# Optimization experiments

Measured on AMD Instinct MI355X. Metric: run time of the kernel, lower is better.

The kernel has to match this reference:

```python
import jax, jax.numpy as jnp
import numpy as np

B, T, D, H = 8, 2048, 512, 2048
EPS = 1e-5


def setup_inputs() -> dict:
    key = jax.random.key(0)
    ks = jax.random.split(key, 12)
    s_d = 1.0 / np.sqrt(D)
    s_h = 1.0 / np.sqrt(H)
    s_w = np.sqrt(6.0 / (T + T))  # xavier_uniform scale for w [T,T]
    return {
        "x": jax.random.normal(ks[0], (B, T, D), jnp.float32),
        "ln1_g": jnp.ones((D,), jnp.float32),
        "ln1_b": jnp.zeros((D,), jnp.float32),
        "Wk": jax.random.normal(ks[1], (D, D), jnp.float32) * s_d,
        "bk": jnp.zeros((D,), jnp.float32),
        "Wv": jax.random.normal(ks[2], (D, D), jnp.float32) * s_d,
        "bv": jnp.zeros((D,), jnp.float32),
        "Wq": jax.random.normal(ks[3], (D, D), jnp.float32) * s_d,
        "bq": jnp.zeros((D,), jnp.float32),
        "w": jax.random.uniform(ks[4], (T, T), jnp.float32, -s_w, s_w),
        "Wo": jax.random.normal(ks[5], (D, D), jnp.float32) * s_d,
        "bo": jnp.zeros((D,), jnp.float32),
        "ln2_g": jnp.ones((D,), jnp.float32),
        "ln2_b": jnp.zeros((D,), jnp.float32),
        "W1": jax.random.normal(ks[6], (D, H), jnp.float32) * s_d,
        "b1": jnp.zeros((H,), jnp.float32),
        "W2": jax.random.normal(ks[7], (H, D), jnp.float32) * s_h,
        "b2": jnp.zeros((D,), jnp.float32),
    }


def _ln(x, g, b):
    mu = jnp.mean(x, axis=-1, keepdims=True)
    var = jnp.mean(jnp.square(x - mu), axis=-1, keepdims=True)
    return (x - mu) * jax.lax.rsqrt(var + EPS) * g + b


def _aft_full(h, Wk, bk, Wv, bv, Wq, bq, w, Wo, bo):
    # h: [B,T,D]
    K = h @ Wk + bk
    V = h @ Wv + bv
    # row-max stabilized position bias [T,T]
    exp_w = jnp.exp(w - jnp.max(w, axis=-1, keepdims=True))
    # NOTE: original stabilizes K with max over dim=0 (the BATCH dim) -- faithful
    exp_K = jnp.exp(K - jnp.max(K, axis=0, keepdims=True))  # [B,T,D]
    num = jnp.einsum("ts,bsd->btd", exp_w, exp_K * V)
    den = jnp.einsum("ts,bsd->btd", exp_w, exp_K)
    Yt = num / den
    Q = h @ Wq + bq
    Yt = jax.nn.sigmoid(Q) * Yt
    return Yt @ Wo + bo


def reference(x, ln1_g, ln1_b, Wk, bk, Wv, bv, Wq, bq, w, Wo, bo,
              ln2_g, ln2_b, W1, b1, W2, b2):
    attn = _aft_full(_ln(x, ln1_g, ln1_b), Wk, bk, Wv, bv, Wq, bq, w, Wo, bo)
    out = attn + x
    h = _ln(out, ln2_g, ln2_b)
    h = jax.nn.gelu(h @ W1 + b1, approximate=False)
    h = jax.nn.gelu(h @ W2 + b2, approximate=False)  # GELU after 2nd linear too (faithful)
    return h + out
```

## Files before the change

### kernel.cpp

```cpp
#include <hip/hip_runtime.h>
#include <hip/hip_bf16.h>
#include <math.h>

typedef __hip_bfloat16 bf16;
typedef __bf16 bf16x8 __attribute__((ext_vector_type(8)));
typedef float f32x4 __attribute__((ext_vector_type(4)));

#define B_ 8
#define T_ 2048
#define D_ 512
#define H_ 2048

__device__ __forceinline__ float b2f(unsigned short u) {
    return __uint_as_float((unsigned)u << 16);
}
__device__ __forceinline__ float ldf(const float* p, long i) { return p[i]; }
__device__ __forceinline__ float ldf(const bf16* p, long i) {
    return b2f(((const unsigned short*)p)[i]);
}
__device__ __forceinline__ float gelu_f(float v) {
    float a = 1.5957691216057308f * (v + 0.044715f * v * v * v);
    return v / (1.0f + __expf(-a));
}

__device__ __forceinline__ long poff(int row, int col, int K) {
    return ((long)(row >> 4) * (K >> 5) + (col >> 5)) * 512 + (row & 15) * 32 + (col & 31);
}

#define GLD16(g, l)                                                          \
    __builtin_amdgcn_global_load_lds(                                        \
        (const __attribute__((address_space(1))) void*)(g),                  \
        (__attribute__((address_space(3))) void*)(l), 16, 0, 0)

template <typename Tin, bool PACKO>
__global__ __launch_bounds__(256) void ln_kernel(const Tin* __restrict__ x,
                                                 const float* __restrict__ g,
                                                 const float* __restrict__ bb,
                                                 bf16* __restrict__ y) {
    int row = blockIdx.x;
    long base = (long)row * D_;
    int tid = threadIdx.x;
    float v0 = ldf(x, base + tid);
    float v1 = ldf(x, base + tid + 256);
    float s = v0 + v1;
#pragma unroll
    for (int off = 32; off > 0; off >>= 1) s += __shfl_down(s, off);
    __shared__ float red[4];
    int lane = tid & 63, wid = tid >> 6;
    if (lane == 0) red[wid] = s;
    __syncthreads();
    float mean = (red[0] + red[1] + red[2] + red[3]) * (1.0f / 512.0f);
    __syncthreads();
    float d0 = v0 - mean, d1 = v1 - mean;
    float vs = d0 * d0 + d1 * d1;
#pragma unroll
    for (int off = 32; off > 0; off >>= 1) vs += __shfl_down(vs, off);
    if (lane == 0) red[wid] = vs;
    __syncthreads();
    float var = (red[0] + red[1] + red[2] + red[3]) * (1.0f / 512.0f);
    float rstd = rsqrtf(var + 1e-5f);
    float o0 = d0 * rstd * g[tid] + bb[tid];
    float o1 = d1 * rstd * g[tid + 256] + bb[tid + 256];
    if (PACKO) {
        y[poff(row, tid, D_)]       = __float2bfloat16(o0);
        y[poff(row, tid + 256, D_)] = __float2bfloat16(o1);
    } else {
        y[base + tid]       = __float2bfloat16(o0);
        y[base + tid + 256] = __float2bfloat16(o1);
    }
}

__global__ __launch_bounds__(256) void expw_kernel(const float* __restrict__ w,
                                                   bf16* __restrict__ ew) {
    int row = blockIdx.x;
    long base = (long)row * T_;
    int tid = threadIdx.x;
    float v[8];
    float mx = -3.4e38f;
#pragma unroll
    for (int i = 0; i < 8; ++i) {
        v[i] = w[base + tid + i * 256];
        mx = fmaxf(mx, v[i]);
    }
#pragma unroll
    for (int off = 32; off > 0; off >>= 1) mx = fmaxf(mx, __shfl_down(mx, off));
    __shared__ float red[4];
    if ((tid & 63) == 0) red[tid >> 6] = mx;
    __syncthreads();
    float rmax = fmaxf(fmaxf(red[0], red[1]), fmaxf(red[2], red[3]));
#pragma unroll
    for (int i = 0; i < 8; ++i)
        ew[poff(row, tid + i * 256, T_)] = __float2bfloat16(expf(v[i] - rmax));
}

__global__ __launch_bounds__(256) void maxk_kernel(const bf16* __restrict__ K,
                                                   float* __restrict__ mk) {
    long i = (long)blockIdx.x * 256 + threadIdx.x;
    float m = ldf(K, i);
#pragma unroll
    for (int b = 1; b < B_; ++b) m = fmaxf(m, ldf(K, (long)b * (T_ * D_) + i));
    mk[i] = m;
}

__global__ __launch_bounds__(256) void kv2t_kernel(const bf16* __restrict__ K_,
                                                   const bf16* __restrict__ V_,
                                                   const float* __restrict__ mk,
                                                   bf16* __restrict__ kv2t) {
    __shared__ float sev[64][65];
    __shared__ float se[64][65];
    int tx = threadIdx.x & 63, ty = threadIdx.x >> 6;
    int t0 = blockIdx.x * 64, d0 = blockIdx.y * 64, b = blockIdx.z;
    long ibase = (long)b << 20;
#pragma unroll
    for (int r = 0; r < 16; ++r) {
        int tl = r * 4 + ty;
        long mi = (long)(t0 + tl) * D_ + d0 + tx;
        float e = expf(ldf(K_, ibase + mi) - mk[mi]);
        sev[tl][tx] = e * ldf(V_, ibase + mi);
        se[tl][tx] = e;
    }
    __syncthreads();
    long obase = (long)b << 21;
#pragma unroll
    for (int r = 0; r < 16; ++r) {
        int dl = r * 4 + ty;
        kv2t[obase + poff(d0 + dl, t0 + tx, T_)]       = __float2bfloat16(sev[tx][dl]);
        kv2t[obase + poff(512 + d0 + dl, t0 + tx, T_)] = __float2bfloat16(se[tx][dl]);
    }
}

__global__ __launch_bounds__(256) void yt_kernel(const bf16* __restrict__ nd,
                                                 bf16* __restrict__ q) {
    long i = (long)blockIdx.x * 256 + threadIdx.x;
    long td = i & (long)(T_ * D_ - 1);
    long b = i >> 20;
    long t = td >> 9;
    long d = td & (D_ - 1);
    long base = (b << 21) + (t << 10);
    float num = ldf(nd, base + d), den = ldf(nd, base + D_ + d);
    q[i] = __float2bfloat16(ldf(q, i) * num / den);
}

struct WT6 {
    const float* src[6];
    bf16* dst[6];
    int K[6], N[6];
};
__global__ __launch_bounds__(256) void wtrans6_kernel(WT6 p) {
    int z = blockIdx.z;
    int K = p.K[z], N = p.N[z];
    int n0 = blockIdx.x * 64, k0 = blockIdx.y * 64;
    if (n0 >= N || k0 >= K) return;
    const float* W = p.src[z];
    bf16* WT = p.dst[z];
    __shared__ float s[64][65];
    int tx = threadIdx.x & 63, ty = threadIdx.x >> 6;
#pragma unroll
    for (int r = 0; r < 16; ++r) {
        int kl = r * 4 + ty;
        s[kl][tx] = W[(long)(k0 + kl) * N + n0 + tx];
    }
    __syncthreads();
#pragma unroll
    for (int r = 0; r < 16; ++r) {
        int nl = r * 4 + ty;
        WT[poff(n0 + nl, k0 + tx, K)] = __float2bfloat16(s[tx][nl]);
    }
}

template <int BM, int PK>
__global__ __launch_bounds__(256, 4) void mfma_gemm(
    const bf16* __restrict__ A, const bf16* __restrict__ Bt,
    const float* __restrict__ b0, const float* __restrict__ b1,
    const float* __restrict__ b2,
    bf16* __restrict__ Cb, float* __restrict__ Cf,
    const bf16* __restrict__ resb, const float* __restrict__ resf,
    int M, int N, int K, int modes, long bsB, long bsC, long planeStride) {
    constexpr int MI = BM / 32;
    constexpr int NA = BM / 64;
    constexpr int PL = (BM + 128) * 32;
    constexpr bool PA = PK & 1, PB = PK & 2, PCK = PK & 4;
    constexpr long astep = PA ? 512 : 32;
    constexpr long bstep = PB ? 512 : 32;
    __shared__ short Sh[2 * PL];
    int tid = threadIdx.x;
    int lane = tid & 63, wave = tid >> 6;
    int wm = wave & 1, wn = wave >> 1;

    int gx = gridDim.x, gy = gridDim.y;
    long nwg = (long)gx * gy * gridDim.z;
    long o = blockIdx.x + (long)gx * (blockIdx.y + (long)gy * blockIdx.z);
    long wk = (o & 7) * (nwg >> 3) + (o >> 3);
    int bx = (int)(wk % gx);
    long rq = wk / gx;
    int by = (int)(rq % gy);
    int bz = (int)(rq / gy);
    int m0 = by * BM, n0 = bx * 128;

    const short* Ag = (const short*)A;
    const short* Bg = (const short*)Bt + (long)bz * bsB;

    int lr = lane >> 2;
    int le = (lane & 3) * 8;
    const short* ga[NA];
    short* la[NA];
#pragma unroll
    for (int i = 0; i < NA; ++i) {
        int arow = m0 + wave * (BM / 4) + i * 16;
        ga[i] = PA ? Ag + (long)(arow >> 4) * ((long)K << 4) + lane * 8
                   : Ag + (long)(arow + lr) * K + le;
        la[i] = Sh + (wave * (BM / 4) + i * 16) * 32;
    }
    int brow = n0 + wave * 32;
    const short* gb0 = PB ? Bg + (long)(brow >> 4) * ((long)K << 4) + lane * 8
                          : Bg + (long)(brow + lr) * K + le;
    const short* gb1 = PB ? gb0 + ((long)K << 4) : gb0 + 16L * K;
    short* lb0 = Sh + BM * 32 + (wave * 32) * 32;
    short* lb1 = lb0 + 16 * 32;

    f32x4 acc[MI][4];
    f32x4 zz = {0.f, 0.f, 0.f, 0.f};
#pragma unroll
    for (int i = 0; i < MI; ++i)
#pragma unroll
        for (int j = 0; j < 4; ++j) acc[i][j] = zz;

    int fr = lane & 15;
    int fk = (lane >> 4) * 8;
    int rm = wm * (BM / 2);

    auto stage = [&](int kt, int ofs) {
#pragma unroll
        for (int i = 0; i < NA; ++i) GLD16(ga[i] + kt * astep, la[i] + ofs);
        GLD16(gb0 + kt * bstep, lb0 + ofs);
        GLD16(gb1 + kt * bstep, lb1 + ofs);
    };
    auto compute = [&](int ofs) {
        const short* Asb = Sh + ofs;
        const short* Bsb = Sh + ofs + BM * 32;
        bf16x8 af[MI], bv[4];
#pragma unroll
        for (int mi = 0; mi < MI; ++mi)
            af[mi] = *(const bf16x8*)(Asb + (rm + mi * 16 + fr) * 32 + fk);
#pragma unroll
        for (int ni = 0; ni < 4; ++ni)
            bv[ni] = *(const bf16x8*)(Bsb + (wn * 64 + ni * 16 + fr) * 32 + fk);
#pragma unroll
        for (int mi = 0; mi < MI; ++mi)
#pragma unroll
            for (int ni = 0; ni < 4; ++ni)
                acc[mi][ni] = __builtin_amdgcn_mfma_f32_16x16x32_bf16(
                    af[mi], bv[ni], acc[mi][ni], 0, 0, 0);
    };

    int nk = K >> 5;
    stage(0, 0);
    __syncthreads();
    for (int kt = 0; kt < nk; kt += 2) {
        if (kt + 1 < nk) stage(kt + 1, PL);
        compute(0);
        __syncthreads();
        if (kt + 2 < nk) stage(kt + 2, 0);
        compute(PL);
        __syncthreads();
    }

    int cc = lane & 15, cr = (lane >> 4) * 4;
    long cbase = (long)bz * bsC;
#pragma unroll
    for (int mi = 0; mi < MI; ++mi) {
#pragma unroll
        for (int ni = 0; ni < 4; ++ni) {
            int row0 = m0 + rm + mi * 16 + cr;
            int col = n0 + wn * 64 + ni * 16 + cc;
            float bvl;
            long colterm;
            int md, rowstride;
            if (planeStride) {
                int plane = col >> 9;
                int c2 = col & 511;
                const float* bp = (plane == 0) ? b0 : ((plane == 1) ? b1 : b2);
                bvl = bp[c2];
                md = (modes >> (2 * plane)) & 3;
                colterm = (long)plane * planeStride + c2;
                rowstride = 512;
            } else {
                bvl = b0 ? b0[col] : 0.0f;
                md = modes & 3;
                colterm = col;
                rowstride = N;
            }
#pragma unroll
            for (int r = 0; r < 4; ++r) {
                float v = acc[mi][ni][r] + bvl;
                if (md == 1) v = 1.0f / (1.0f + __expf(-v));
                else if (md == 2) v = gelu_f(v);
                long idx;
                if (PCK) idx = cbase + poff(row0 + r, col, N);
                else     idx = cbase + (long)(row0 + r) * rowstride + colterm;
                if (resf) v += resf[idx];
                if (resb) v += ldf(resb, idx);
                if (Cf) Cf[idx] = v;
                else Cb[idx] = __float2bfloat16(v);
            }
        }
    }
}

extern "C" void kernel_launch(void* const* d_in, const int* in_sizes, int n_in,
                              void* d_out, int out_size, void* d_ws, size_t ws_size,
                              hipStream_t stream) {
    const float* x    = (const float*)d_in[0];
    const float* ln1g = (const float*)d_in[1];
    const float* ln1b = (const float*)d_in[2];
    const float* Wk   = (const float*)d_in[3];
    const float* bk   = (const float*)d_in[4];
    const float* Wv   = (const float*)d_in[5];
    const float* bv   = (const float*)d_in[6];
    const float* Wq   = (const float*)d_in[7];
    const float* bq   = (const float*)d_in[8];
    const float* w    = (const float*)d_in[9];
    const float* Wo   = (const float*)d_in[10];
    const float* bo   = (const float*)d_in[11];
    const float* ln2g = (const float*)d_in[12];
    const float* ln2b = (const float*)d_in[13];
    const float* W1   = (const float*)d_in[14];
    const float* b1   = (const float*)d_in[15];
    const float* W2   = (const float*)d_in[16];
    const float* b2   = (const float*)d_in[17];
    float* out = (float*)d_out;

    const long S_BTD = (long)B_ * T_ * D_;
    const long S_TD  = (long)T_ * D_;
    const long S_TT  = (long)T_ * T_;
    const long S_B2D = (long)B_ * T_ * 2 * D_;
    const long S_DD  = (long)D_ * D_;

    bf16* h1     = (bf16*)d_ws;
    bf16* outres = h1 + S_BTD;
    bf16* ew     = outres + S_BTD;
    bf16* KVQ    = ew + S_TT;
    bf16* kv2t   = KVQ + 3 * S_BTD;
    float* mk    = (float*)(kv2t + S_B2D);
    bf16* WkT    = (bf16*)(mk + S_TD);
    bf16* WvT    = WkT + S_DD;
    bf16* WqT    = WvT + S_DD;
    bf16* WoT    = WqT + S_DD;
    bf16* W1T    = WoT + S_DD;
    bf16* W2T    = W1T + (long)D_ * H_;
    bf16* Kb  = KVQ;
    bf16* Vb  = KVQ + S_BTD;
    bf16* Qb  = KVQ + 2 * S_BTD;
    bf16* nd  = KVQ;
    bf16* hH  = KVQ;
    bf16* h2  = h1;

    const int M = B_ * T_;

    WT6 p;
    p.src[0] = Wk; p.src[1] = Wv; p.src[2] = Wq; p.src[3] = Wo; p.src[4] = W1; p.src[5] = W2;
    p.dst[0] = WkT; p.dst[1] = WvT; p.dst[2] = WqT; p.dst[3] = WoT; p.dst[4] = W1T; p.dst[5] = W2T;
    p.K[0] = p.K[1] = p.K[2] = p.K[3] = 512; p.K[4] = 512; p.K[5] = 2048;
    p.N[0] = p.N[1] = p.N[2] = p.N[3] = 512; p.N[4] = 2048; p.N[5] = 512;
    wtrans6_kernel<<<dim3(32, 32, 6), 256, 0, stream>>>(p);
    ln_kernel<float, true><<<M, 256, 0, stream>>>(x, ln1g, ln1b, h1);
    mfma_gemm<128, 3><<<dim3(1536 / 128, M / 128, 1), 256, 0, stream>>>(
        h1, WkT, bk, bv, bq, Kb, nullptr, nullptr, nullptr,
        M, 1536, D_, (1 << 4), 0, 0, S_BTD);
    maxk_kernel<<<S_TD / 256, 256, 0, stream>>>(Kb, mk);
    kv2t_kernel<<<dim3(T_ / 64, D_ / 64, B_), 256, 0, stream>>>(Kb, Vb, mk, kv2t);
    expw_kernel<<<T_, 256, 0, stream>>>(w, ew);
    mfma_gemm<128, 3><<<dim3(1024 / 128, T_ / 128, B_), 256, 0, stream>>>(
        ew, kv2t, nullptr, nullptr, nullptr, nd, nullptr, nullptr, nullptr,
        T_, 1024, T_, 0, (long)1024 * T_, (long)T_ * 1024, 0);
    yt_kernel<<<S_BTD / 256, 256, 0, stream>>>(nd, Qb);
    mfma_gemm<128, 2><<<dim3(D_ / 128, M / 128, 1), 256, 0, stream>>>(
        Qb, WoT, bo, nullptr, nullptr, outres, nullptr, nullptr, x,
        M, D_, D_, 0, 0, 0, 0);
    ln_kernel<bf16, true><<<M, 256, 0, stream>>>(outres, ln2g, ln2b, h2);
    mfma_gemm<128, 7><<<dim3(H_ / 128, M / 128, 1), 256, 0, stream>>>(
        h2, W1T, b1, nullptr, nullptr, hH, nullptr, nullptr, nullptr,
        M, H_, D_, 2, 0, 0, 0);
    mfma_gemm<128, 3><<<dim3(D_ / 128, M / 128, 1), 256, 0, stream>>>(
        hH, W2T, b2, nullptr, nullptr, nullptr, out, outres, nullptr,
        M, D_, H_, 2, 0, 0, 0);
}
```

Before: 473.9 us.

## Load MFMA fragments directly from packed global memory, bypassing LDS staging

Adds an NL variant of the GEMM that reads bf16x8 fragments straight from the 16x32-packed global layout into registers, skipping shared-memory staging and barriers. It is used for the dense linear GEMMs, while the AFT einsum GEMM keeps the LDS double buffer. The QKV/Wo outputs now use the packed layout, so kv2t and yt index into packed tiles. The cost is that data reuse between waves now depends on L1/L2 instead of LDS, and there is no explicit prefetch, so latency may be exposed.

Result: slower. 624.4 us (+31.7%).

```diff
diff --git a/kernel.cpp b/kernel.cpp
--- a/kernel.cpp
+++ b/kernel.cpp
@@ -114,9 +114,9 @@
 #pragma unroll
     for (int r = 0; r < 16; ++r) {
         int tl = r * 4 + ty;
-        long mi = (long)(t0 + tl) * D_ + d0 + tx;
-        float e = expf(ldf(K_, ibase + mi) - mk[mi]);
-        sev[tl][tx] = e * ldf(V_, ibase + mi);
+        long pi = poff(t0 + tl, d0 + tx, D_);
+        float e = expf(ldf(K_, ibase + pi) - mk[pi]);
+        sev[tl][tx] = e * ldf(V_, ibase + pi);
         se[tl][tx] = e;
     }
     __syncthreads();
@@ -132,12 +132,15 @@
 __global__ __launch_bounds__(256) void yt_kernel(const bf16* __restrict__ nd,
                                                  bf16* __restrict__ q) {
     long i = (long)blockIdx.x * 256 + threadIdx.x;
-    long td = i & (long)(T_ * D_ - 1);
     long b = i >> 20;
-    long t = td >> 9;
-    long d = td & (D_ - 1);
-    long base = (b << 21) + (t << 10);
-    float num = ldf(nd, base + d), den = ldf(nd, base + D_ + d);
+    long p = i & (long)(T_ * D_ - 1);
+    int tile = (int)(p >> 9);
+    int ro = (int)((p >> 5) & 15);
+    int cs = (int)(p & 31);
+    int t = (tile >> 4) * 16 + ro;
+    int d = (tile & 15) * 32 + cs;
+    long base = (b << 21) + ((long)t << 10);
+    float num = ldf(nd, base + d), den = ldf(nd, base + 512 + d);
     q[i] = __float2bfloat16(ldf(q, i) * num / den);
 }
 
@@ -168,8 +171,8 @@
     }
 }
 
-template <int BM, int PK>
-__global__ __launch_bounds__(256, 4) void mfma_gemm(
+template <int BM, bool NL, int PCK>
+__global__ __launch_bounds__(256, NL ? 3 : 4) void mfma_gemm(
     const bf16* __restrict__ A, const bf16* __restrict__ Bt,
     const float* __restrict__ b0, const float* __restrict__ b1,
     const float* __restrict__ b2,
@@ -179,10 +182,7 @@
     constexpr int MI = BM / 32;
     constexpr int NA = BM / 64;
     constexpr int PL = (BM + 128) * 32;
-    constexpr bool PA = PK & 1, PB = PK & 2, PCK = PK & 4;
-    constexpr long astep = PA ? 512 : 32;
-    constexpr long bstep = PB ? 512 : 32;
-    __shared__ short Sh[2 * PL];
+    __shared__ short Sh[NL ? 16 : 2 * PL];
     int tid = threadIdx.x;
     int lane = tid & 63, wave = tid >> 6;
     int wm = wave & 1, wn = wave >> 1;
@@ -200,69 +200,90 @@
     const short* Ag = (const short*)A;
     const short* Bg = (const short*)Bt + (long)bz * bsB;
 
-    int lr = lane >> 2;
-    int le = (lane & 3) * 8;
-    const short* ga[NA];
-    short* la[NA];
-#pragma unroll
-    for (int i = 0; i < NA; ++i) {
-        int arow = m0 + wave * (BM / 4) + i * 16;
-        ga[i] = PA ? Ag + (long)(arow >> 4) * ((long)K << 4) + lane * 8
-                   : Ag + (long)(arow + lr) * K + le;
-        la[i] = Sh + (wave * (BM / 4) + i * 16) * 32;
-    }
-    int brow = n0 + wave * 32;
-    const short* gb0 = PB ? Bg + (long)(brow >> 4) * ((long)K << 4) + lane * 8
-                          : Bg + (long)(brow + lr) * K + le;
-    const short* gb1 = PB ? gb0 + ((long)K << 4) : gb0 + 16L * K;
-    short* lb0 = Sh + BM * 32 + (wave * 32) * 32;
-    short* lb1 = lb0 + 16 * 32;
-
-    f32x4 acc[MI][4];
-    f32x4 zz = {0.f, 0.f, 0.f, 0.f};
-#pragma unroll
-    for (int i = 0; i < MI; ++i)
-#pragma unroll
-        for (int j = 0; j < 4; ++j) acc[i][j] = zz;
-
     int fr = lane & 15;
     int fk = (lane >> 4) * 8;
     int rm = wm * (BM / 2);
 
-    auto stage = [&](int kt, int ofs) {
-#pragma unroll
-        for (int i = 0; i < NA; ++i) GLD16(ga[i] + kt * astep, la[i] + ofs);
-        GLD16(gb0 + kt * bstep, lb0 + ofs);
-        GLD16(gb1 + kt * bstep, lb1 + ofs);
-    };
-    auto compute = [&](int ofs) {
-        const short* Asb = Sh + ofs;
-        const short* Bsb = Sh + ofs + BM * 32;
-        bf16x8 af[MI], bv[4];
-#pragma unroll
-        for (int mi = 0; mi < MI; ++mi)
-            af[mi] = *(const bf16x8*)(Asb + (rm + mi * 16 + fr) * 32 + fk);
-#pragma unroll
-        for (int ni = 0; ni < 4; ++ni)
-            bv[ni] = *(const bf16x8*)(Bsb + (wn * 64 + ni * 16 + fr) * 32 + fk);
-#pragma unroll
-        for (int mi = 0; mi < MI; ++mi)
+    f32x4 acc[MI][4];
+    f32x4 zz = {0.f, 0.f, 0.f, 0.f};
+#pragma unroll
+    for (int i = 0; i < MI; ++i)
+#pragma unroll
+        for (int j = 0; j < 4; ++j) acc[i][j] = zz;
+
+    if constexpr (NL) {
+        const long ts = (long)K << 4;
+        const int lo = fr * 32 + fk;
+        const short* Aw = Ag + (long)((m0 >> 4) + wm * MI) * ts + lo;
+        const short* Bw = Bg + (long)((n0 >> 4) + wn * 4) * ts + lo;
+        int nk = K >> 5;
+#pragma unroll 2
+        for (int kt = 0; kt < nk; ++kt) {
+            bf16x8 af[MI], bv[4];
+            long ko = (long)kt * 512;
+#pragma unroll
+            for (int mi = 0; mi < MI; ++mi)
+                af[mi] = *(const bf16x8*)(Aw + (long)mi * ts + ko);
 #pragma unroll
             for (int ni = 0; ni < 4; ++ni)
-                acc[mi][ni] = __builtin_amdgcn_mfma_f32_16x16x32_bf16(
-                    af[mi], bv[ni], acc[mi][ni], 0, 0, 0);
-    };
-
-    int nk = K >> 5;
-    stage(0, 0);
-    __syncthreads();
-    for (int kt = 0; kt < nk; kt += 2) {
-        if (kt + 1 < nk) stage(kt + 1, PL);
-        compute(0);
+                bv[ni] = *(const bf16x8*)(Bw + (long)ni * ts + ko);
+#pragma unroll
+            for (int mi = 0; mi < MI; ++mi)
+#pragma unroll
+                for (int ni = 0; ni < 4; ++ni)
+                    acc[mi][ni] = __builtin_amdgcn_mfma_f32_16x16x32_bf16(
+                        af[mi], bv[ni], acc[mi][ni], 0, 0, 0);
+        }
+    } else {
+        const short* ga[NA];
+        short* la[NA];
+#pragma unroll
+        for (int i = 0; i < NA; ++i) {
+            int arow = m0 + wave * (BM / 4) + i * 16;
+            ga[i] = Ag + (long)(arow >> 4) * ((long)K << 4) + lane * 8;
+            la[i] = Sh + (wave * (BM / 4) + i * 16) * 32;
+        }
+        int brow = n0 + wave * 32;
+        const short* gb0 = Bg + (long)(brow >> 4) * ((long)K << 4) + lane * 8;
+        const short* gb1 = gb0 + ((long)K << 4);
+        short* lb0 = Sh + BM * 32 + (wave * 32) * 32;
+        short* lb1 = lb0 + 16 * 32;
+
+        auto stage = [&](int kt, int ofs) {
+#pragma unroll
+            for (int i = 0; i < NA; ++i) GLD16(ga[i] + (long)kt * 512, la[i] + ofs);
+            GLD16(gb0 + (long)kt * 512, lb0 + ofs);
+            GLD16(gb1 + (long)kt * 512, lb1 + ofs);
+        };
+        auto compute = [&](int ofs) {
+            const short* Asb = Sh + ofs;
+            const short* Bsb = Sh + ofs + BM * 32;
+            bf16x8 af[MI], bv[4];
+#pragma unroll
+            for (int mi = 0; mi < MI; ++mi)
+                af[mi] = *(const bf16x8*)(Asb + (rm + mi * 16 + fr) * 32 + fk);
+#pragma unroll
+            for (int ni = 0; ni < 4; ++ni)
+                bv[ni] = *(const bf16x8*)(Bsb + (wn * 64 + ni * 16 + fr) * 32 + fk);
+#pragma unroll
+            for (int mi = 0; mi < MI; ++mi)
+#pragma unroll
+                for (int ni = 0; ni < 4; ++ni)
+                    acc[mi][ni] = __builtin_amdgcn_mfma_f32_16x16x32_bf16(
+                        af[mi], bv[ni], acc[mi][ni], 0, 0, 0);
+        };
+
+        int nk = K >> 5;
+        stage(0, 0);
         __syncthreads();
-        if (kt + 2 < nk) stage(kt + 2, 0);
-        compute(PL);
-        __syncthreads();
+        for (int kt = 0; kt < nk; kt += 2) {
+            if (kt + 1 < nk) stage(kt + 1, PL);
+            compute(0);
+            __syncthreads();
+            if (kt + 2 < nk) stage(kt + 2, 0);
+            compute(PL);
+            __syncthreads();
+        }
     }
 
     int cc = lane & 15, cr = (lane >> 4) * 4;
@@ -274,21 +295,17 @@
             int row0 = m0 + rm + mi * 16 + cr;
             int col = n0 + wn * 64 + ni * 16 + cc;
             float bvl;
-            long colterm;
-            int md, rowstride;
+            int md;
+            int plane = 0, c2 = col;
             if (planeStride) {
-                int plane = col >> 9;
-                int c2 = col & 511;
+                plane = col >> 9;
+                c2 = col & 511;
                 const float* bp = (plane == 0) ? b0 : ((plane == 1) ? b1 : b2);
                 bvl = bp[c2];
                 md = (modes >> (2 * plane)) & 3;
-                colterm = (long)plane * planeStride + c2;
-                rowstride = 512;
             } else {
                 bvl = b0 ? b0[col] : 0.0f;
                 md = modes & 3;
-                colterm = col;
-                rowstride = N;
             }
 #pragma unroll
             for (int r = 0; r < 4; ++r) {
@@ -296,8 +313,9 @@
                 if (md == 1) v = 1.0f / (1.0f + __expf(-v));
                 else if (md == 2) v = gelu_f(v);
                 long idx;
-                if (PCK) idx = cbase + poff(row0 + r, col, N);
-                else     idx = cbase + (long)(row0 + r) * rowstride + colterm;
+                if (planeStride) idx = (long)plane * planeStride + poff(row0 + r, c2, 512);
+                else if (PCK)    idx = cbase + poff(row0 + r, col, N);
+                else             idx = cbase + (long)(row0 + r) * N + col;
                 if (resf) v += resf[idx];
                 if (resb) v += ldf(resb, idx);
                 if (Cf) Cf[idx] = v;
@@ -364,24 +382,24 @@
     p.N[0] = p.N[1] = p.N[2] = p.N[3] = 512; p.N[4] = 2048; p.N[5] = 512;
     wtrans6_kernel<<<dim3(32, 32, 6), 256, 0, stream>>>(p);
     ln_kernel<float, true><<<M, 256, 0, stream>>>(x, ln1g, ln1b, h1);
-    mfma_gemm<128, 3><<<dim3(1536 / 128, M / 128, 1), 256, 0, stream>>>(
+    mfma_gemm<128, true, 0><<<dim3(1536 / 128, M / 128, 1), 256, 0, stream>>>(
         h1, WkT, bk, bv, bq, Kb, nullptr, nullptr, nullptr,
         M, 1536, D_, (1 << 4), 0, 0, S_BTD);
     maxk_kernel<<<S_TD / 256, 256, 0, stream>>>(Kb, mk);
     kv2t_kernel<<<dim3(T_ / 64, D_ / 64, B_), 256, 0, stream>>>(Kb, Vb, mk, kv2t);
     expw_kernel<<<T_, 256, 0, stream>>>(w, ew);
-    mfma_gemm<128, 3><<<dim3(1024 / 128, T_ / 128, B_), 256, 0, stream>>>(
+    mfma_gemm<128, false, 0><<<dim3(1024 / 128, T_ / 128, B_), 256, 0, stream>>>(
         ew, kv2t, nullptr, nullptr, nullptr, nd, nullptr, nullptr, nullptr,
         T_, 1024, T_, 0, (long)1024 * T_, (long)T_ * 1024, 0);
     yt_kernel<<<S_BTD / 256, 256, 0, stream>>>(nd, Qb);
-    mfma_gemm<128, 2><<<dim3(D_ / 128, M / 128, 1), 256, 0, stream>>>(
+    mfma_gemm<128, true, 0><<<dim3(D_ / 128, M / 128, 1), 256, 0, stream>>>(
         Qb, WoT, bo, nullptr, nullptr, outres, nullptr, nullptr, x,
         M, D_, D_, 0, 0, 0, 0);
     ln_kernel<bf16, true><<<M, 256, 0, stream>>>(outres, ln2g, ln2b, h2);
-    mfma_gemm<128, 7><<<dim3(H_ / 128, M / 128, 1), 256, 0, stream>>>(
+    mfma_gemm<128, true, 4><<<dim3(H_ / 128, M / 128, 1), 256, 0, stream>>>(
         h2, W1T, b1, nullptr, nullptr, hH, nullptr, nullptr, nullptr,
         M, H_, D_, 2, 0, 0, 0);
-    mfma_gemm<128, 3><<<dim3(D_ / 128, M / 128, 1), 256, 0, stream>>>(
+    mfma_gemm<128, true, 0><<<dim3(D_ / 128, M / 128, 1), 256, 0, stream>>>(
         hH, W2T, b2, nullptr, nullptr, nullptr, out, outres, nullptr,
         M, D_, H_, 2, 0, 0, 0);
 }
```

## Load weight B-fragments directly from global memory, bypassing LDS, in weight GEMMs

Applied to the files above, without the earlier changes.

Adds a BD template mode to the MFMA GEMM. In the weight-projection GEMMs, the packed B (weight) fragments are read straight from global memory into registers instead of being staged through LDS. This halves the LDS footprint per block and removes the B staging traffic. The risk is global-load latency sitting on the MFMA critical path, since these loads are not double-buffered. The per-column K max is also stored as bf16 instead of fp32, which shrinks that buffer but loses some precision in the stabiliser.

Measured after the change: 509.8 us. +7.6%, slower.

```diff
diff --git a/kernel.cpp b/kernel.cpp
--- a/kernel.cpp
+++ b/kernel.cpp
@@ -94,17 +94,17 @@
 }
 
 __global__ __launch_bounds__(256) void maxk_kernel(const bf16* __restrict__ K,
-                                                   float* __restrict__ mk) {
+                                                   bf16* __restrict__ mk) {
     long i = (long)blockIdx.x * 256 + threadIdx.x;
     float m = ldf(K, i);
 #pragma unroll
     for (int b = 1; b < B_; ++b) m = fmaxf(m, ldf(K, (long)b * (T_ * D_) + i));
-    mk[i] = m;
+    mk[i] = __float2bfloat16(m);
 }
 
 __global__ __launch_bounds__(256) void kv2t_kernel(const bf16* __restrict__ K_,
                                                    const bf16* __restrict__ V_,
-                                                   const float* __restrict__ mk,
+                                                   const bf16* __restrict__ mk,
                                                    bf16* __restrict__ kv2t) {
     __shared__ float sev[64][65];
     __shared__ float se[64][65];
@@ -115,7 +115,7 @@
     for (int r = 0; r < 16; ++r) {
         int tl = r * 4 + ty;
         long mi = (long)(t0 + tl) * D_ + d0 + tx;
-        float e = expf(ldf(K_, ibase + mi) - mk[mi]);
+        float e = expf(ldf(K_, ibase + mi) - ldf(mk, mi));
         sev[tl][tx] = e * ldf(V_, ibase + mi);
         se[tl][tx] = e;
     }
@@ -168,7 +168,7 @@
     }
 }
 
-template <int BM, int PK>
+template <int BM, int PK, int BD>
 __global__ __launch_bounds__(256, 4) void mfma_gemm(
     const bf16* __restrict__ A, const bf16* __restrict__ Bt,
     const float* __restrict__ b0, const float* __restrict__ b1,
@@ -178,11 +178,12 @@
     int M, int N, int K, int modes, long bsB, long bsC, long planeStride) {
     constexpr int MI = BM / 32;
     constexpr int NA = BM / 64;
-    constexpr int PL = (BM + 128) * 32;
+    constexpr int PLL = BD ? BM * 32 : (BM + 128) * 32;
     constexpr bool PA = PK & 1, PB = PK & 2, PCK = PK & 4;
+    static_assert(!BD || PB, "BD requires packed B");
     constexpr long astep = PA ? 512 : 32;
     constexpr long bstep = PB ? 512 : 32;
-    __shared__ short Sh[2 * PL];
+    __shared__ short Sh[2 * PLL];
     int tid = threadIdx.x;
     int lane = tid & 63, wave = tid >> 6;
     int wm = wave & 1, wn = wave >> 1;
@@ -211,40 +212,51 @@
                    : Ag + (long)(arow + lr) * K + le;
         la[i] = Sh + (wave * (BM / 4) + i * 16) * 32;
     }
-    int brow = n0 + wave * 32;
-    const short* gb0 = PB ? Bg + (long)(brow >> 4) * ((long)K << 4) + lane * 8
-                          : Bg + (long)(brow + lr) * K + le;
-    const short* gb1 = PB ? gb0 + ((long)K << 4) : gb0 + 16L * K;
-    short* lb0 = Sh + BM * 32 + (wave * 32) * 32;
-    short* lb1 = lb0 + 16 * 32;
-
-    f32x4 acc[MI][4];
-    f32x4 zz = {0.f, 0.f, 0.f, 0.f};
-#pragma unroll
-    for (int i = 0; i < MI; ++i)
-#pragma unroll
-        for (int j = 0; j < 4; ++j) acc[i][j] = zz;
 
     int fr = lane & 15;
     int fk = (lane >> 4) * 8;
     int rm = wm * (BM / 2);
 
+    const long ts = (long)K << 4;
+    const short* Bw = Bg + (long)((n0 >> 4) + wn * 4) * ts + fr * 32 + fk;
+    int brow = n0 + wave * 32;
+    const short* gb0 = PB ? Bg + (long)(brow >> 4) * ts + lane * 8
+                          : Bg + (long)(brow + lr) * K + le;
+    const short* gb1 = PB ? gb0 + ts : gb0 + 16L * K;
+    short* lb0 = Sh + BM * 32 + (wave * 32) * 32;
+    short* lb1 = lb0 + 16 * 32;
+
+    f32x4 acc[MI][4];
+    f32x4 zz = {0.f, 0.f, 0.f, 0.f};
+#pragma unroll
+    for (int i = 0; i < MI; ++i)
+#pragma unroll
+        for (int j = 0; j < 4; ++j) acc[i][j] = zz;
+
     auto stage = [&](int kt, int ofs) {
 #pragma unroll
         for (int i = 0; i < NA; ++i) GLD16(ga[i] + kt * astep, la[i] + ofs);
-        GLD16(gb0 + kt * bstep, lb0 + ofs);
-        GLD16(gb1 + kt * bstep, lb1 + ofs);
+        if constexpr (!BD) {
+            GLD16(gb0 + kt * bstep, lb0 + ofs);
+            GLD16(gb1 + kt * bstep, lb1 + ofs);
+        }
     };
-    auto compute = [&](int ofs) {
+    auto compute = [&](int ofs, int kt) {
         const short* Asb = Sh + ofs;
-        const short* Bsb = Sh + ofs + BM * 32;
         bf16x8 af[MI], bv[4];
 #pragma unroll
         for (int mi = 0; mi < MI; ++mi)
             af[mi] = *(const bf16x8*)(Asb + (rm + mi * 16 + fr) * 32 + fk);
-#pragma unroll
-        for (int ni = 0; ni < 4; ++ni)
-            bv[ni] = *(const bf16x8*)(Bsb + (wn * 64 + ni * 16 + fr) * 32 + fk);
+        if constexpr (BD) {
+#pragma unroll
+            for (int ni = 0; ni < 4; ++ni)
+                bv[ni] = *(const bf16x8*)(Bw + (long)ni * ts + (long)kt * 512);
+        } else {
+            const short* Bsb = Sh + ofs + BM * 32;
+#pragma unroll
+            for (int ni = 0; ni < 4; ++ni)
+                bv[ni] = *(const bf16x8*)(Bsb + (wn * 64 + ni * 16 + fr) * 32 + fk);
+        }
 #pragma unroll
         for (int mi = 0; mi < MI; ++mi)
 #pragma unroll
@@ -257,11 +269,11 @@
     stage(0, 0);
     __syncthreads();
     for (int kt = 0; kt < nk; kt += 2) {
-        if (kt + 1 < nk) stage(kt + 1, PL);
-        compute(0);
+        if (kt + 1 < nk) stage(kt + 1, PLL);
+        compute(0, kt);
         __syncthreads();
         if (kt + 2 < nk) stage(kt + 2, 0);
-        compute(PL);
+        compute(PLL, kt + 1);
         __syncthreads();
     }
 
@@ -341,8 +353,8 @@
     bf16* ew     = outres + S_BTD;
     bf16* KVQ    = ew + S_TT;
     bf16* kv2t   = KVQ + 3 * S_BTD;
-    float* mk    = (float*)(kv2t + S_B2D);
-    bf16* WkT    = (bf16*)(mk + S_TD);
+    bf16* mk     = kv2t + S_B2D;
+    bf16* WkT    = mk + 2 * S_TD;
     bf16* WvT    = WkT + S_DD;
     bf16* WqT    = WvT + S_DD;
     bf16* WoT    = WqT + S_DD;
@@ -364,24 +376,24 @@
     p.N[0] = p.N[1] = p.N[2] = p.N[3] = 512; p.N[4] = 2048; p.N[5] = 512;
     wtrans6_kernel<<<dim3(32, 32, 6), 256, 0, stream>>>(p);
     ln_kernel<float, true><<<M, 256, 0, stream>>>(x, ln1g, ln1b, h1);
-    mfma_gemm<128, 3><<<dim3(1536 / 128, M / 128, 1), 256, 0, stream>>>(
+    mfma_gemm<128, 3, 1><<<dim3(1536 / 128, M / 128, 1), 256, 0, stream>>>(
         h1, WkT, bk, bv, bq, Kb, nullptr, nullptr, nullptr,
         M, 1536, D_, (1 << 4), 0, 0, S_BTD);
     maxk_kernel<<<S_TD / 256, 256, 0, stream>>>(Kb, mk);
     kv2t_kernel<<<dim3(T_ / 64, D_ / 64, B_), 256, 0, stream>>>(Kb, Vb, mk, kv2t);
     expw_kernel<<<T_, 256, 0, stream>>>(w, ew);
-    mfma_gemm<128, 3><<<dim3(1024 / 128, T_ / 128, B_), 256, 0, stream>>>(
+    mfma_gemm<128, 3, 0><<<dim3(1024 / 128, T_ / 128, B_), 256, 0, stream>>>(
         ew, kv2t, nullptr, nullptr, nullptr, nd, nullptr, nullptr, nullptr,
         T_, 1024, T_, 0, (long)1024 * T_, (long)T_ * 1024, 0);
     yt_kernel<<<S_BTD / 256, 256, 0, stream>>>(nd, Qb);
-    mfma_gemm<128, 2><<<dim3(D_ / 128, M / 128, 1), 256, 0, stream>>>(
+    mfma_gemm<128, 2, 1><<<dim3(D_ / 128, M / 128, 1), 256, 0, stream>>>(
         Qb, WoT, bo, nullptr, nullptr, outres, nullptr, nullptr, x,
         M, D_, D_, 0, 0, 0, 0);
     ln_kernel<bf16, true><<<M, 256, 0, stream>>>(outres, ln2g, ln2b, h2);
-    mfma_gemm<128, 7><<<dim3(H_ / 128, M / 128, 1), 256, 0, stream>>>(
+    mfma_gemm<128, 7, 1><<<dim3(H_ / 128, M / 128, 1), 256, 0, stream>>>(
         h2, W1T, b1, nullptr, nullptr, hH, nullptr, nullptr, nullptr,
         M, H_, D_, 2, 0, 0, 0);
-    mfma_gemm<128, 3><<<dim3(D_ / 128, M / 128, 1), 256, 0, stream>>>(
+    mfma_gemm<128, 3, 1><<<dim3(D_ / 128, M / 128, 1), 256, 0, stream>>>(
         hH, W2T, b2, nullptr, nullptr, nullptr, out, outres, nullptr,
         M, D_, H_, 2, 0, 0, 0);
 }
```

## Fuse num/den division and sigmoid-Q gating into AFT GEMM epilogue

Applied to the files above, without the earlier changes.

Interleaves numerator and denominator rows in the kv2t operand so each adjacent column pair of the AFT GEMM output holds num and den for one feature. The GEMM epilogue then divides them with a lane shuffle, multiplies by the stored sigmoid(Q) and writes the result in place. This removes the yt_kernel launch and the round trip of the nd intermediate through memory. It also stores the per-position K max in bf16 instead of fp32 to halve that buffer's traffic, at some cost in precision. Half the lanes sit idle in the new epilogue and their bf16 stores are strided.

Measured after the change: 486.4 us. 2.6% more time.

```diff
diff --git a/kernel.cpp b/kernel.cpp
--- a/kernel.cpp
+++ b/kernel.cpp
@@ -94,17 +94,17 @@
 }
 
 __global__ __launch_bounds__(256) void maxk_kernel(const bf16* __restrict__ K,
-                                                   float* __restrict__ mk) {
+                                                   bf16* __restrict__ mk) {
     long i = (long)blockIdx.x * 256 + threadIdx.x;
     float m = ldf(K, i);
 #pragma unroll
     for (int b = 1; b < B_; ++b) m = fmaxf(m, ldf(K, (long)b * (T_ * D_) + i));
-    mk[i] = m;
+    mk[i] = __float2bfloat16(m);
 }
 
 __global__ __launch_bounds__(256) void kv2t_kernel(const bf16* __restrict__ K_,
                                                    const bf16* __restrict__ V_,
-                                                   const float* __restrict__ mk,
+                                                   const bf16* __restrict__ mk,
                                                    bf16* __restrict__ kv2t) {
     __shared__ float sev[64][65];
     __shared__ float se[64][65];
@@ -115,7 +115,7 @@
     for (int r = 0; r < 16; ++r) {
         int tl = r * 4 + ty;
         long mi = (long)(t0 + tl) * D_ + d0 + tx;
-        float e = expf(ldf(K_, ibase + mi) - mk[mi]);
+        float e = expf(ldf(K_, ibase + mi) - ldf(mk, mi));
         sev[tl][tx] = e * ldf(V_, ibase + mi);
         se[tl][tx] = e;
     }
@@ -124,21 +124,10 @@
 #pragma unroll
     for (int r = 0; r < 16; ++r) {
         int dl = r * 4 + ty;
-        kv2t[obase + poff(d0 + dl, t0 + tx, T_)]       = __float2bfloat16(sev[tx][dl]);
-        kv2t[obase + poff(512 + d0 + dl, t0 + tx, T_)] = __float2bfloat16(se[tx][dl]);
-    }
-}
-
-__global__ __launch_bounds__(256) void yt_kernel(const bf16* __restrict__ nd,
-                                                 bf16* __restrict__ q) {
-    long i = (long)blockIdx.x * 256 + threadIdx.x;
-    long td = i & (long)(T_ * D_ - 1);
-    long b = i >> 20;
-    long t = td >> 9;
-    long d = td & (D_ - 1);
-    long base = (b << 21) + (t << 10);
-    float num = ldf(nd, base + d), den = ldf(nd, base + D_ + d);
-    q[i] = __float2bfloat16(ldf(q, i) * num / den);
+        int nrow = 2 * (d0 + dl);
+        kv2t[obase + poff(nrow,     t0 + tx, T_)] = __float2bfloat16(sev[tx][dl]);
+        kv2t[obase + poff(nrow + 1, t0 + tx, T_)] = __float2bfloat16(se[tx][dl]);
+    }
 }
 
 struct WT6 {
@@ -175,6 +164,7 @@
     const float* __restrict__ b2,
     bf16* __restrict__ Cb, float* __restrict__ Cf,
     const bf16* __restrict__ resb, const float* __restrict__ resf,
+    bf16* __restrict__ yq,
     int M, int N, int K, int modes, long bsB, long bsC, long planeStride) {
     constexpr int MI = BM / 32;
     constexpr int NA = BM / 64;
@@ -266,6 +256,29 @@
     }
 
     int cc = lane & 15, cr = (lane >> 4) * 4;
+    if (yq) {
+        long qb = (long)bz * (long)(T_ * D_);
+#pragma unroll
+        for (int mi = 0; mi < MI; ++mi) {
+#pragma unroll
+            for (int ni = 0; ni < 4; ++ni) {
+                int row0 = m0 + rm + mi * 16 + cr;
+                int col = n0 + wn * 64 + ni * 16 + cc;
+                int d = col >> 1;
+#pragma unroll
+                for (int r = 0; r < 4; ++r) {
+                    float v = acc[mi][ni][r];
+                    float other = __shfl_xor(v, 1);
+                    if (!(lane & 1)) {
+                        long qi = qb + (long)(row0 + r) * D_ + d;
+                        float sq = ldf((const bf16*)yq, qi);
+                        yq[qi] = __float2bfloat16(sq * v / other);
+                    }
+                }
+            }
+        }
+        return;
+    }
     long cbase = (long)bz * bsC;
 #pragma unroll
     for (int mi = 0; mi < MI; ++mi) {
@@ -341,8 +354,8 @@
     bf16* ew     = outres + S_BTD;
     bf16* KVQ    = ew + S_TT;
     bf16* kv2t   = KVQ + 3 * S_BTD;
-    float* mk    = (float*)(kv2t + S_B2D);
-    bf16* WkT    = (bf16*)(mk + S_TD);
+    bf16* mk     = kv2t + S_B2D;
+    bf16* WkT    = mk + 2 * S_TD;
     bf16* WvT    = WkT + S_DD;
     bf16* WqT    = WvT + S_DD;
     bf16* WoT    = WqT + S_DD;
@@ -351,7 +364,6 @@
     bf16* Kb  = KVQ;
     bf16* Vb  = KVQ + S_BTD;
     bf16* Qb  = KVQ + 2 * S_BTD;
-    bf16* nd  = KVQ;
     bf16* hH  = KVQ;
     bf16* h2  = h1;
 
@@ -365,23 +377,22 @@
     wtrans6_kernel<<<dim3(32, 32, 6), 256, 0, stream>>>(p);
     ln_kernel<float, true><<<M, 256, 0, stream>>>(x, ln1g, ln1b, h1);
     mfma_gemm<128, 3><<<dim3(1536 / 128, M / 128, 1), 256, 0, stream>>>(
-        h1, WkT, bk, bv, bq, Kb, nullptr, nullptr, nullptr,
+        h1, WkT, bk, bv, bq, Kb, nullptr, nullptr, nullptr, nullptr,
         M, 1536, D_, (1 << 4), 0, 0, S_BTD);
     maxk_kernel<<<S_TD / 256, 256, 0, stream>>>(Kb, mk);
     kv2t_kernel<<<dim3(T_ / 64, D_ / 64, B_), 256, 0, stream>>>(Kb, Vb, mk, kv2t);
     expw_kernel<<<T_, 256, 0, stream>>>(w, ew);
     mfma_gemm<128, 3><<<dim3(1024 / 128, T_ / 128, B_), 256, 0, stream>>>(
-        ew, kv2t, nullptr, nullptr, nullptr, nd, nullptr, nullptr, nullptr,
-        T_, 1024, T_, 0, (long)1024 * T_, (long)T_ * 1024, 0);
-    yt_kernel<<<S_BTD / 256, 256, 0, stream>>>(nd, Qb);
+        ew, kv2t, nullptr, nullptr, nullptr, nullptr, nullptr, nullptr, nullptr, Qb,
+        T_, 1024, T_, 0, (long)1024 * T_, 0, 0);
     mfma_gemm<128, 2><<<dim3(D_ / 128, M / 128, 1), 256, 0, stream>>>(
-        Qb, WoT, bo, nullptr, nullptr, outres, nullptr, nullptr, x,
+        Qb, WoT, bo, nullptr, nullptr, outres, nullptr, nullptr, x, nullptr,
         M, D_, D_, 0, 0, 0, 0);
     ln_kernel<bf16, true><<<M, 256, 0, stream>>>(outres, ln2g, ln2b, h2);
     mfma_gemm<128, 7><<<dim3(H_ / 128, M / 128, 1), 256, 0, stream>>>(
-        h2, W1T, b1, nullptr, nullptr, hH, nullptr, nullptr, nullptr,
+        h2, W1T, b1, nullptr, nullptr, hH, nullptr, nullptr, nullptr, nullptr,
         M, H_, D_, 2, 0, 0, 0);
     mfma_gemm<128, 3><<<dim3(D_ / 128, M / 128, 1), 256, 0, stream>>>(
-        hH, W2T, b2, nullptr, nullptr, nullptr, out, outres, nullptr,
+        hH, W2T, b2, nullptr, nullptr, nullptr, out, outres, nullptr, nullptr,
         M, D_, H_, 2, 0, 0, 0);
 }
```
